# Optimization experiments

Hardware: AMD Instinct MI355X
Metric: run time of the kernel (lower is better)

Reference implementation:

```python
import jax, jax.numpy as jnp
import numpy as np

NUM_HEADS = 16


def setup_inputs() -> dict:
    key = jax.random.key(0)
    ks = jax.random.split(key, 3)
    S, B, E = 2048, 4, 1024
    query = jax.random.normal(ks[0], (S, B, E), dtype=jnp.float32)
    # xavier-uniform-ish scale for projection weights
    w_in = jax.random.normal(ks[1], (3 * E, E), dtype=jnp.float32) * (1.0 / np.sqrt(E))
    b_in = jnp.zeros((3 * E,), dtype=jnp.float32)
    w_out = jax.random.normal(ks[2], (E, E), dtype=jnp.float32) * (1.0 / np.sqrt(E))
    b_out = jnp.zeros((E,), dtype=jnp.float32)
    return {"query": query, "w_in": w_in, "b_in": b_in, "w_out": w_out, "b_out": b_out}


def reference(query, w_in, b_in, w_out, b_out):
    # query: [S, B, E] (seq-first, like nn.MultiheadAttention)
    S, B, E = query.shape
    H = NUM_HEADS
    D = E // H
    scaling = float(D) ** -0.5

    # fused in-projection: [S, B, 3E]
    P = jnp.einsum('sbe,fe->sbf', query, w_in) + b_in
    q, k, v = jnp.split(P, 3, axis=-1)
    q = q * scaling

    # split heads -> [S, B, H, D]
    q = q.reshape(S, B, H, D)
    k = k.reshape(S, B, H, D)
    v = v.reshape(S, B, H, D)

    # scores: [B, H, S(tgt), S(src)] — full O(S^2) matrix, as in the original
    scores = jnp.einsum('sbhd,tbhd->bhst', q, k)
    attn = jax.nn.softmax(scores, axis=-1)  # dropout_p = 0.0

    # context: [S, B, H, D] -> [S, B, E]
    ctx = jnp.einsum('bhst,tbhd->sbhd', attn, v).reshape(S, B, E)

    # out projection
    out = jnp.einsum('sbe,fe->sbf', ctx, w_out) + b_out
    return out
```

## Files before the change

### kernel.cpp

```cpp
#include <hip/hip_runtime.h>
#include <hip/hip_bf16.h>

#define SQ  2048
#define NB  4
#define EE  1024
#define NH  16
#define DH  64
#define BH  64
#define MROWS 8192

using bf16x8 = __attribute__((ext_vector_type(8))) short;
using f32x4  = __attribute__((ext_vector_type(4))) float;

#define MFMA16(a,b,c) __builtin_amdgcn_mfma_f32_16x16x32_bf16((a),(b),(c),0,0,0)

__device__ __forceinline__ short f2bf(float f) {
  union { float f; unsigned u; } v; v.f = f;
  unsigned r = (v.u + 0x7FFFu + ((v.u >> 16) & 1u)) >> 16;
  return (short)r;
}

__device__ __forceinline__ void gload_lds16(const void* g, void* l) {
  __builtin_amdgcn_global_load_lds((__attribute__((address_space(1))) void*)(g),
                                   (__attribute__((address_space(3))) void*)(l),
                                   16, 0, 0);
}

__global__ __launch_bounds__(256) void cvt_f32_bf16(const float* __restrict__ src,
                                                    short* __restrict__ dst, int n4) {
  int i = blockIdx.x * 256 + threadIdx.x;
  int stride = gridDim.x * 256;
  for (; i < n4; i += stride) {
    float4 v = reinterpret_cast<const float4*>(src)[i];
    short4 o;
    o.x = f2bf(v.x); o.y = f2bf(v.y); o.z = f2bf(v.z); o.w = f2bf(v.w);
    reinterpret_cast<short4*>(dst)[i] = o;
  }
}

template<int MODE>
__global__ __launch_bounds__(256) void gemm_bt(const short* __restrict__ A,
                                               const short* __restrict__ B,
                                               const float* __restrict__ bias,
                                               short* __restrict__ obf,
                                               float* __restrict__ of,
                                               int M, int N, int K) {
  __shared__ short As[128 * 64];
  __shared__ short Bs[128 * 64];
  const int tid  = threadIdx.x;
  const int wave = tid >> 6, lane = tid & 63;
  const int g = lane >> 4, qc = lane & 15;
  const int wr = wave >> 1, wc = wave & 1;
  const int m0 = blockIdx.y << 7, n0 = blockIdx.x << 7;

  f32x4 acc[4][4];
  const f32x4 z4 = {0.f, 0.f, 0.f, 0.f};
#pragma unroll
  for (int m = 0; m < 4; ++m)
#pragma unroll
    for (int n = 0; n < 4; ++n) acc[m][n] = z4;

  const int KT = K >> 6;
  for (int kt = 0; kt < KT; ++kt) {
    const int k0 = kt << 6;
    __syncthreads();
#pragma unroll
    for (int ro = 0; ro < 4; ++ro) {
      int slot = ro * 256 + tid;
      int row  = slot >> 3;
      int cb   = (slot & 7) << 4;
      gload_lds16((const char*)A + ((size_t)(m0 + row) * K + k0) * 2 + cb,
                  (char*)As + ro * 4096 + wave * 1024);
      gload_lds16((const char*)B + ((size_t)(n0 + row) * K + k0) * 2 + cb,
                  (char*)Bs + ro * 4096 + wave * 1024);
    }
    __syncthreads();
#pragma unroll
    for (int kk = 0; kk < 2; ++kk) {
      bf16x8 af[4], bfr[4];
#pragma unroll
      for (int m = 0; m < 4; ++m)
        af[m] = *(const bf16x8*)&As[(wr * 64 + m * 16 + qc) * 64 + kk * 32 + g * 8];
#pragma unroll
      for (int n = 0; n < 4; ++n)
        bfr[n] = *(const bf16x8*)&Bs[(wc * 64 + n * 16 + qc) * 64 + kk * 32 + g * 8];
#pragma unroll
      for (int m = 0; m < 4; ++m)
#pragma unroll
        for (int n = 0; n < 4; ++n)
          acc[m][n] = MFMA16(af[m], bfr[n], acc[m][n]);
    }
  }

#pragma unroll
  for (int m = 0; m < 4; ++m) {
#pragma unroll
    for (int n = 0; n < 4; ++n) {
#pragma unroll
      for (int r = 0; r < 4; ++r) {
        int R = m0 + wr * 64 + m * 16 + 4 * g + r;
        int F = n0 + wc * 64 + n * 16 + qc;
        float val = acc[m][n][r] + bias[F];
        if (MODE == 0) {
          int qkv = F >> 10, e = F & 1023;
          if (qkv == 0) val *= 0.125f;
          int h = e >> 6, d = e & 63;
          int s = R >> 2, b = R & 3;
          obf[(size_t)(((qkv << 6) + (b << 4) + h) * SQ + s) * DH + d] = f2bf(val);
        } else {
          of[(size_t)R * N + F] = val;
        }
      }
    }
  }
}

__global__ __launch_bounds__(256) void transpose_v(const short* __restrict__ V,
                                                   short* __restrict__ Vt) {
  __shared__ short T[64 * 72];
  const int bh = blockIdx.y, s0 = blockIdx.x << 6;
  const int tid = threadIdx.x;
  const size_t base = (size_t)bh * SQ * DH;
#pragma unroll
  for (int ro = 0; ro < 2; ++ro) {
    int slot = ro * 256 + tid;
    int row  = slot >> 3;
    int c8   = (slot & 7) << 3;
    bf16x8 v = *(const bf16x8*)(V + base + (size_t)(s0 + row) * DH + c8);
#pragma unroll
    for (int j = 0; j < 8; ++j) T[(c8 + j) * 72 + row] = v[j];
  }
  __syncthreads();
#pragma unroll
  for (int ro = 0; ro < 2; ++ro) {
    int slot = ro * 256 + tid;
    int row  = slot >> 3;
    int c8   = (slot & 7) << 3;
    bf16x8 v = *(const bf16x8*)&T[row * 72 + c8];
    *(bf16x8*)(Vt + base + (size_t)row * SQ + s0 + c8) = v;
  }
}

__global__ __launch_bounds__(256) void attn(const short* __restrict__ Q,
                                            const short* __restrict__ K,
                                            const short* __restrict__ Vt,
                                            short* __restrict__ ctx) {
  __shared__ short Ks[64 * 72];
  __shared__ short Vs[64 * 72];
  __shared__ short Ps[4][16 * 72];
  const int bh = blockIdx.y;
  const int q0 = blockIdx.x << 6;
  const int tid = threadIdx.x;
  const int wave = tid >> 6, lane = tid & 63;
  const int g = lane >> 4, qc = lane & 15;
  const size_t base = (size_t)bh * SQ * DH;

  bf16x8 qf0, qf1;
  {
    const short* qr = Q + base + (size_t)(q0 + wave * 16 + qc) * DH;
    qf0 = *(const bf16x8*)(qr + g * 8);
    qf1 = *(const bf16x8*)(qr + 32 + g * 8);
  }

  const f32x4 z4 = {0.f, 0.f, 0.f, 0.f};
  f32x4 acc[4];
#pragma unroll
  for (int dt = 0; dt < 4; ++dt) acc[dt] = z4;
  float mrun = -3e38f, lrun = 0.f;

  for (int kt = 0; kt < SQ / 64; ++kt) {
    const int kv0 = kt << 6;
    __syncthreads();
#pragma unroll
    for (int ro = 0; ro < 2; ++ro) {
      int slot = ro * 256 + tid;
      int row  = slot >> 3;
      int c8   = (slot & 7) << 3;
      bf16x8 kv_ = *(const bf16x8*)(K + base + (size_t)(kv0 + row) * DH + c8);
      *(bf16x8*)&Ks[row * 72 + c8] = kv_;
      bf16x8 vv_ = *(const bf16x8*)(Vt + base + (size_t)row * SQ + kv0 + c8);
      *(bf16x8*)&Vs[row * 72 + c8] = vv_;
    }
    __syncthreads();

    f32x4 sc[4];
#pragma unroll
    for (int t = 0; t < 4; ++t) {
      bf16x8 kf0 = *(const bf16x8*)&Ks[(t * 16 + qc) * 72 + g * 8];
      bf16x8 kf1 = *(const bf16x8*)&Ks[(t * 16 + qc) * 72 + 32 + g * 8];
      f32x4 z = z4;
      z = MFMA16(kf0, qf0, z);
      z = MFMA16(kf1, qf1, z);
      sc[t] = z;
    }

    float pmax = -3e38f;
#pragma unroll
    for (int t = 0; t < 4; ++t)
#pragma unroll
      for (int r = 0; r < 4; ++r) pmax = fmaxf(pmax, sc[t][r]);
    pmax = fmaxf(pmax, __shfl_xor(pmax, 16));
    pmax = fmaxf(pmax, __shfl_xor(pmax, 32));
    float mnew  = fmaxf(mrun, pmax);
    float alpha = __expf(mrun - mnew);
    float psum = 0.f;
#pragma unroll
    for (int t = 0; t < 4; ++t) {
      float p0 = __expf(sc[t][0] - mnew);
      float p1 = __expf(sc[t][1] - mnew);
      float p2 = __expf(sc[t][2] - mnew);
      float p3 = __expf(sc[t][3] - mnew);
      psum += (p0 + p1) + (p2 + p3);
      uint2 w;
      w.x = (unsigned)(unsigned short)f2bf(p0) | ((unsigned)(unsigned short)f2bf(p1) << 16);
      w.y = (unsigned)(unsigned short)f2bf(p2) | ((unsigned)(unsigned short)f2bf(p3) << 16);
      *(uint2*)&Ps[wave][qc * 72 + t * 16 + g * 4] = w;
    }
    psum += __shfl_xor(psum, 16);
    psum += __shfl_xor(psum, 32);
    lrun = lrun * alpha + psum;
    mrun = mnew;

    float a_r[4];
#pragma unroll
    for (int r = 0; r < 4; ++r) a_r[r] = __shfl(alpha, 4 * g + r);
#pragma unroll
    for (int dt = 0; dt < 4; ++dt) {
      acc[dt][0] *= a_r[0]; acc[dt][1] *= a_r[1];
      acc[dt][2] *= a_r[2]; acc[dt][3] *= a_r[3];
    }

    bf16x8 pa0 = *(const bf16x8*)&Ps[wave][qc * 72 + g * 8];
    bf16x8 pa1 = *(const bf16x8*)&Ps[wave][qc * 72 + 32 + g * 8];
#pragma unroll
    for (int dt = 0; dt < 4; ++dt) {
      bf16x8 vf0 = *(const bf16x8*)&Vs[(dt * 16 + qc) * 72 + g * 8];
      bf16x8 vf1 = *(const bf16x8*)&Vs[(dt * 16 + qc) * 72 + 32 + g * 8];
      acc[dt] = MFMA16(pa0, vf0, acc[dt]);
      acc[dt] = MFMA16(pa1, vf1, acc[dt]);
    }
  }

  float linv = 1.f / lrun;
  float l_r[4];
#pragma unroll
  for (int r = 0; r < 4; ++r) l_r[r] = __shfl(linv, 4 * g + r);
  const int b_ = bh >> 4, h = bh & 15;
#pragma unroll
  for (int dt = 0; dt < 4; ++dt) {
#pragma unroll
    for (int r = 0; r < 4; ++r) {
      int s = q0 + wave * 16 + 4 * g + r;
      int e = h * 64 + dt * 16 + qc;
      ctx[(size_t)(s * 4 + b_) * EE + e] = f2bf(acc[dt][r] * l_r[r]);
    }
  }
}

extern "C" void kernel_launch(void* const* d_in, const int* in_sizes, int n_in,
                              void* d_out, int out_size, void* d_ws, size_t ws_size,
                              hipStream_t stream) {
  const float* query = (const float*)d_in[0];
  const float* w_in  = (const float*)d_in[1];
  const float* b_in  = (const float*)d_in[2];
  const float* w_out = (const float*)d_in[3];
  const float* b_out = (const float*)d_in[4];
  float* out = (float*)d_out;

  char* ws = (char*)d_ws;
  short* Xbf  = (short*)(ws);
  short* Wbf  = (short*)(ws + (size_t)(16 << 20));
  short* WObf = (short*)(ws + (size_t)(22 << 20));
  short* QKV  = (short*)(ws + (size_t)(24 << 20));
  short* Vt   = (short*)(ws + (size_t)(72 << 20));
  short* ctx  = Xbf;

  cvt_f32_bf16<<<1024, 256, 0, stream>>>(query, Xbf, (SQ * NB * EE) / 4);
  cvt_f32_bf16<<<512, 256, 0, stream>>>(w_in, Wbf, (3 * EE * EE) / 4);
  cvt_f32_bf16<<<256, 256, 0, stream>>>(w_out, WObf, (EE * EE) / 4);

  gemm_bt<0><<<dim3(24, 64), 256, 0, stream>>>(Xbf, Wbf, b_in, QKV, nullptr,
                                               MROWS, 3 * EE, EE);
  transpose_v<<<dim3(32, 64), 256, 0, stream>>>(QKV + 2 * (size_t)8388608, Vt);
  attn<<<dim3(32, 64), 256, 0, stream>>>(QKV, QKV + (size_t)8388608, Vt, ctx);
  gemm_bt<1><<<dim3(8, 64), 256, 0, stream>>>(ctx, WObf, b_out, nullptr, out,
                                              MROWS, EE, EE);
}
```

Before: 374.4 us.

## Double query rows per wave, prefetch K/V via registers, use exp2 with lazy rescale

The attention kernel now processes 128 query rows per block (32 per wave), so each K/V tile loaded into shared memory serves twice as many queries and the grid halves. The next K/V tile is prefetched into registers while the current one is computed. Softmax folds log2(e) into the Q scaling so exp2f can be used, and it skips the accumulator rescale when the running max grows by no more than a threshold. Bf16 packing now uses the hardware v_cvt_pk_bf16_f32 instruction. The cost is more registers per thread and fewer blocks, which may lower occupancy.

```diff
diff --git a/kernel.cpp b/kernel.cpp
--- a/kernel.cpp
+++ b/kernel.cpp
@@ -18,6 +18,12 @@
   union { float f; unsigned u; } v; v.f = f;
   unsigned r = (v.u + 0x7FFFu + ((v.u >> 16) & 1u)) >> 16;
   return (short)r;
+}
+
+__device__ __forceinline__ unsigned cvtpk_bf16(float lo, float hi) {
+  unsigned r;
+  asm("v_cvt_pk_bf16_f32 %0, %1, %2" : "=v"(r) : "v"(lo), "v"(hi));
+  return r;
 }
 
 __device__ __forceinline__ void gload_lds16(const void* g, void* l) {
@@ -103,7 +109,7 @@
         float val = acc[m][n][r] + bias[F];
         if (MODE == 0) {
           int qkv = F >> 10, e = F & 1023;
-          if (qkv == 0) val *= 0.125f;
+          if (qkv == 0) val *= 0.18033688011112042f;
           int h = e >> 6, d = e & 63;
           int s = R >> 2, b = R & 3;
           obf[(size_t)(((qkv << 6) + (b << 4) + h) * SQ + s) * DH + d] = f2bf(val);
@@ -147,112 +153,139 @@
                                             short* __restrict__ ctx) {
   __shared__ short Ks[64 * 72];
   __shared__ short Vs[64 * 72];
-  __shared__ short Ps[4][16 * 72];
+  __shared__ short Ps[4][32 * 72];
   const int bh = blockIdx.y;
-  const int q0 = blockIdx.x << 6;
+  const int q0 = blockIdx.x << 7;
   const int tid = threadIdx.x;
   const int wave = tid >> 6, lane = tid & 63;
   const int g = lane >> 4, qc = lane & 15;
   const size_t base = (size_t)bh * SQ * DH;
 
-  bf16x8 qf0, qf1;
-  {
-    const short* qr = Q + base + (size_t)(q0 + wave * 16 + qc) * DH;
-    qf0 = *(const bf16x8*)(qr + g * 8);
-    qf1 = *(const bf16x8*)(qr + 32 + g * 8);
+  bf16x8 qf[2][2];
+#pragma unroll
+  for (int qh = 0; qh < 2; ++qh) {
+    const short* qr = Q + base + (size_t)(q0 + wave * 32 + qh * 16 + qc) * DH;
+    qf[qh][0] = *(const bf16x8*)(qr + g * 8);
+    qf[qh][1] = *(const bf16x8*)(qr + 32 + g * 8);
   }
 
   const f32x4 z4 = {0.f, 0.f, 0.f, 0.f};
-  f32x4 acc[4];
-#pragma unroll
-  for (int dt = 0; dt < 4; ++dt) acc[dt] = z4;
-  float mrun = -3e38f, lrun = 0.f;
-
-  for (int kt = 0; kt < SQ / 64; ++kt) {
-    const int kv0 = kt << 6;
+  f32x4 acc[4][2];
+#pragma unroll
+  for (int dt = 0; dt < 4; ++dt) { acc[dt][0] = z4; acc[dt][1] = z4; }
+  float mrun[2] = {-3e38f, -3e38f}, lrun[2] = {0.f, 0.f};
+
+  bf16x8 kreg[2], vreg[2];
+#define LOADKV(KT_) do { int kv0_ = (KT_) << 6;                                  \
+    _Pragma("unroll")                                                            \
+    for (int ro = 0; ro < 2; ++ro) {                                             \
+      int slot = ro * 256 + tid; int row = slot >> 3; int c8 = (slot & 7) << 3;  \
+      kreg[ro] = *(const bf16x8*)(K + base + (size_t)(kv0_ + row) * DH + c8);    \
+      vreg[ro] = *(const bf16x8*)(Vt + base + (size_t)row * SQ + kv0_ + c8);     \
+    } } while (0)
+
+  LOADKV(0);
+
+  const int NT = SQ / 64;
+  for (int kt = 0; kt < NT; ++kt) {
     __syncthreads();
 #pragma unroll
     for (int ro = 0; ro < 2; ++ro) {
-      int slot = ro * 256 + tid;
-      int row  = slot >> 3;
-      int c8   = (slot & 7) << 3;
-      bf16x8 kv_ = *(const bf16x8*)(K + base + (size_t)(kv0 + row) * DH + c8);
-      *(bf16x8*)&Ks[row * 72 + c8] = kv_;
-      bf16x8 vv_ = *(const bf16x8*)(Vt + base + (size_t)row * SQ + kv0 + c8);
-      *(bf16x8*)&Vs[row * 72 + c8] = vv_;
+      int slot = ro * 256 + tid; int row = slot >> 3; int c8 = (slot & 7) << 3;
+      *(bf16x8*)&Ks[row * 72 + c8] = kreg[ro];
+      *(bf16x8*)&Vs[row * 72 + c8] = vreg[ro];
     }
     __syncthreads();
-
-    f32x4 sc[4];
+    int nx = kt + 1 < NT - 1 ? kt + 1 : NT - 1;
+    LOADKV(nx);
+
+    f32x4 sc[2][4];
 #pragma unroll
     for (int t = 0; t < 4; ++t) {
       bf16x8 kf0 = *(const bf16x8*)&Ks[(t * 16 + qc) * 72 + g * 8];
       bf16x8 kf1 = *(const bf16x8*)&Ks[(t * 16 + qc) * 72 + 32 + g * 8];
-      f32x4 z = z4;
-      z = MFMA16(kf0, qf0, z);
-      z = MFMA16(kf1, qf1, z);
-      sc[t] = z;
-    }
-
-    float pmax = -3e38f;
-#pragma unroll
-    for (int t = 0; t < 4; ++t)
-#pragma unroll
-      for (int r = 0; r < 4; ++r) pmax = fmaxf(pmax, sc[t][r]);
-    pmax = fmaxf(pmax, __shfl_xor(pmax, 16));
-    pmax = fmaxf(pmax, __shfl_xor(pmax, 32));
-    float mnew  = fmaxf(mrun, pmax);
-    float alpha = __expf(mrun - mnew);
-    float psum = 0.f;
-#pragma unroll
-    for (int t = 0; t < 4; ++t) {
-      float p0 = __expf(sc[t][0] - mnew);
-      float p1 = __expf(sc[t][1] - mnew);
-      float p2 = __expf(sc[t][2] - mnew);
-      float p3 = __expf(sc[t][3] - mnew);
-      psum += (p0 + p1) + (p2 + p3);
-      uint2 w;
-      w.x = (unsigned)(unsigned short)f2bf(p0) | ((unsigned)(unsigned short)f2bf(p1) << 16);
-      w.y = (unsigned)(unsigned short)f2bf(p2) | ((unsigned)(unsigned short)f2bf(p3) << 16);
-      *(uint2*)&Ps[wave][qc * 72 + t * 16 + g * 4] = w;
-    }
-    psum += __shfl_xor(psum, 16);
-    psum += __shfl_xor(psum, 32);
-    lrun = lrun * alpha + psum;
-    mrun = mnew;
-
-    float a_r[4];
-#pragma unroll
-    for (int r = 0; r < 4; ++r) a_r[r] = __shfl(alpha, 4 * g + r);
-#pragma unroll
-    for (int dt = 0; dt < 4; ++dt) {
-      acc[dt][0] *= a_r[0]; acc[dt][1] *= a_r[1];
-      acc[dt][2] *= a_r[2]; acc[dt][3] *= a_r[3];
-    }
-
-    bf16x8 pa0 = *(const bf16x8*)&Ps[wave][qc * 72 + g * 8];
-    bf16x8 pa1 = *(const bf16x8*)&Ps[wave][qc * 72 + 32 + g * 8];
+      sc[0][t] = MFMA16(kf1, qf[0][1], MFMA16(kf0, qf[0][0], z4));
+      sc[1][t] = MFMA16(kf1, qf[1][1], MFMA16(kf0, qf[1][0], z4));
+    }
+
+#pragma unroll
+    for (int qh = 0; qh < 2; ++qh) {
+      float pmax = -3e38f;
+#pragma unroll
+      for (int t = 0; t < 4; ++t)
+#pragma unroll
+        for (int r = 0; r < 4; ++r) pmax = fmaxf(pmax, sc[qh][t][r]);
+      pmax = fmaxf(pmax, __shfl_xor(pmax, 16));
+      pmax = fmaxf(pmax, __shfl_xor(pmax, 32));
+
+      float mnew = mrun[qh];
+      if (!__all(pmax - mrun[qh] <= 11.0f)) {
+        mnew = fmaxf(mrun[qh], pmax);
+        float alpha = exp2f(mrun[qh] - mnew);
+        float a_r[4];
+#pragma unroll
+        for (int r = 0; r < 4; ++r) a_r[r] = __shfl(alpha, 4 * g + r);
+#pragma unroll
+        for (int dt = 0; dt < 4; ++dt) {
+          acc[dt][qh][0] *= a_r[0]; acc[dt][qh][1] *= a_r[1];
+          acc[dt][qh][2] *= a_r[2]; acc[dt][qh][3] *= a_r[3];
+        }
+        lrun[qh] *= alpha;
+        mrun[qh] = mnew;
+      }
+
+      float psum = 0.f;
+#pragma unroll
+      for (int t = 0; t < 4; ++t) {
+        float p0 = exp2f(sc[qh][t][0] - mnew);
+        float p1 = exp2f(sc[qh][t][1] - mnew);
+        float p2 = exp2f(sc[qh][t][2] - mnew);
+        float p3 = exp2f(sc[qh][t][3] - mnew);
+        psum += (p0 + p1) + (p2 + p3);
+        uint2 w;
+        w.x = cvtpk_bf16(p0, p1);
+        w.y = cvtpk_bf16(p2, p3);
+        *(uint2*)&Ps[wave][(qh * 16 + qc) * 72 + t * 16 + g * 4] = w;
+      }
+      psum += __shfl_xor(psum, 16);
+      psum += __shfl_xor(psum, 32);
+      lrun[qh] += psum;
+    }
+
+    bf16x8 pa[2][2];
+#pragma unroll
+    for (int qh = 0; qh < 2; ++qh) {
+      pa[qh][0] = *(const bf16x8*)&Ps[wave][(qh * 16 + qc) * 72 + g * 8];
+      pa[qh][1] = *(const bf16x8*)&Ps[wave][(qh * 16 + qc) * 72 + 32 + g * 8];
+    }
 #pragma unroll
     for (int dt = 0; dt < 4; ++dt) {
       bf16x8 vf0 = *(const bf16x8*)&Vs[(dt * 16 + qc) * 72 + g * 8];
       bf16x8 vf1 = *(const bf16x8*)&Vs[(dt * 16 + qc) * 72 + 32 + g * 8];
-      acc[dt] = MFMA16(pa0, vf0, acc[dt]);
-      acc[dt] = MFMA16(pa1, vf1, acc[dt]);
-    }
-  }
-
-  float linv = 1.f / lrun;
-  float l_r[4];
-#pragma unroll
-  for (int r = 0; r < 4; ++r) l_r[r] = __shfl(linv, 4 * g + r);
+#pragma unroll
+      for (int qh = 0; qh < 2; ++qh) {
+        acc[dt][qh] = MFMA16(pa[qh][0], vf0, acc[dt][qh]);
+        acc[dt][qh] = MFMA16(pa[qh][1], vf1, acc[dt][qh]);
+      }
+    }
+  }
+#undef LOADKV
+
   const int b_ = bh >> 4, h = bh & 15;
 #pragma unroll
-  for (int dt = 0; dt < 4; ++dt) {
-#pragma unroll
-    for (int r = 0; r < 4; ++r) {
-      int s = q0 + wave * 16 + 4 * g + r;
-      int e = h * 64 + dt * 16 + qc;
-      ctx[(size_t)(s * 4 + b_) * EE + e] = f2bf(acc[dt][r] * l_r[r]);
+  for (int qh = 0; qh < 2; ++qh) {
+    float linv = 1.f / lrun[qh];
+    float l_r[4];
+#pragma unroll
+    for (int r = 0; r < 4; ++r) l_r[r] = __shfl(linv, 4 * g + r);
+#pragma unroll
+    for (int dt = 0; dt < 4; ++dt) {
+#pragma unroll
+      for (int r = 0; r < 4; ++r) {
+        int s = q0 + wave * 32 + qh * 16 + 4 * g + r;
+        int e = h * 64 + dt * 16 + qc;
+        ctx[(size_t)(s * 4 + b_) * EE + e] = f2bf(acc[dt][qh][r] * l_r[r]);
+      }
     }
   }
 }
@@ -282,7 +315,7 @@
   gemm_bt<0><<<dim3(24, 64), 256, 0, stream>>>(Xbf, Wbf, b_in, QKV, nullptr,
                                                MROWS, 3 * EE, EE);
   transpose_v<<<dim3(32, 64), 256, 0, stream>>>(QKV + 2 * (size_t)8388608, Vt);
-  attn<<<dim3(32, 64), 256, 0, stream>>>(QKV, QKV + (size_t)8388608, Vt, ctx);
+  attn<<<dim3(16, 64), 256, 0, stream>>>(QKV, QKV + (size_t)8388608, Vt, ctx);
   gemm_bt<1><<<dim3(8, 64), 256, 0, stream>>>(ctx, WObf, b_out, nullptr, out,
                                               MROWS, EE, EE);
 }
```

Result: faster. 354.8 us (-5.2%).
